# Kernel optimization log

Hardware: AMD Instinct MI355X
Metric: run time of the kernel (lower is better)

The kernel has to match this reference:

```python
import jax, jax.numpy as jnp
import numpy as np

NEG = -1e9  # matches torch masked_fill value -1000000000.0


def setup_inputs() -> dict:
    key = jax.random.key(0)
    ks = jax.random.split(key, 8)
    B, n, m, d = 16, 1024, 128, 768
    C = jax.random.normal(ks[0], (B, n, d), jnp.float32)
    Q = jax.random.normal(ks[1], (B, m, d), jnp.float32)
    c_mask = jax.random.randint(ks[2], (B, 1, n), 0, 2).astype(bool)
    q_mask = jax.random.randint(ks[3], (B, 1, m), 0, 2).astype(bool)
    w1 = jax.random.normal(ks[4], (d,), jnp.float32)
    w2 = jax.random.normal(ks[5], (d,), jnp.float32)
    w3 = jax.random.normal(ks[6], (1, 1, d), jnp.float32)
    bias = jax.random.normal(ks[7], (1, 1), jnp.float32)
    return {"C": C, "Q": Q, "c_mask": c_mask, "q_mask": q_mask,
            "w1": w1, "w2": w2, "w3": w3, "bias": bias}


def reference(C, Q, c_mask, q_mask, w1, w2, w3, bias):
    # trilinear score S[b,i,j] = w1.C_i + w2.Q_j + (C_i * w3) . Q_j
    c_logit = jnp.einsum('bnd,d->bn', C, w1)[:, :, None]      # [B,n,1]
    q_logit = jnp.einsum('bmd,d->bm', Q, w2)[:, None, :]      # [B,1,m]
    dot_logit = jnp.einsum('bnd,bmd->bnm', C * w3, Q)         # [B,n,m]
    S = c_logit + q_logit + dot_logit                          # [B,n,m]

    # C2Q: mask padded query cols and padded context rows, softmax over query dim
    Sm = jnp.where(q_mask, NEG, S)                             # q_mask [B,1,m]
    Sm = jnp.where(jnp.swapaxes(c_mask, 1, 2), NEG, Sm)        # c_mask^T [B,n,1]
    C2Q = jax.nn.softmax(Sm, axis=-1)                          # [B,n,m]

    # Q2C: mask context cols of S^T, max over query dim, softmax over context dim
    St = jnp.where(c_mask, NEG, jnp.swapaxes(S, 1, 2))         # [B,m,n]
    q2c_logits = jnp.max(St, axis=1, keepdims=True)            # [B,1,n]
    Q2C = jax.nn.softmax(q2c_logits, axis=-1)                  # [B,1,n]

    A = jnp.einsum('bnm,bmd->bnd', C2Q, Q)                     # [B,n,d]
    # torch expands Q2C to [B,n,n] then bmm's with C; every row is identical,
    # so compute once and broadcast: [B,1,n] @ [B,n,d] -> [B,1,d]
    Bctx = jnp.einsum('bon,bnd->bod', Q2C, C)                  # [B,1,d]
    Bfull = jnp.broadcast_to(Bctx, C.shape)
    out = jnp.concatenate([C, A, C * A, C * Bfull], axis=-1)   # [B,n,4d]
    return out
```

## Files before the change

kernel.cpp:

```cpp
#include <hip/hip_runtime.h>
#include <math.h>
#include <stdint.h>

#define NEGV -1e9f
typedef float f32x4 __attribute__((ext_vector_type(4)));
typedef short bf16x8 __attribute__((ext_vector_type(8)));
typedef unsigned int u32x4 __attribute__((ext_vector_type(4)));

constexpr int B_ = 16, N_ = 1024, M_ = 128, D_ = 768;
constexpr int NCH = 12;

constexpr size_t OFF_QLOGP  = 0;
constexpr size_t OFF_BCTX   = 98304;
constexpr size_t OFF_PART   = 147456;
constexpr size_t OFF_ROWMAX = 147456;
constexpr size_t OFF_WQ2C   = 212992;
constexpr size_t OFF_PIMG   = 2244608;
constexpr size_t OFF_QIMG   = 10633216;
constexpr size_t SZ_QIMG    = 3145728;
constexpr size_t WS_NEED    = OFF_QIMG + 4 * SZ_QIMG;

__device__ __forceinline__ unsigned short bf_rne(float x) {
    unsigned u = __float_as_uint(x);
    return (unsigned short)((u + 0x7fffu + ((u >> 16) & 1u)) >> 16);
}
__device__ __forceinline__ void splitf(float x, unsigned short& h, unsigned short& l) {
    unsigned short hb = bf_rne(x);
    float hf = __uint_as_float((unsigned)hb << 16);
    h = hb;
    l = bf_rne(x - hf);
}
__device__ __forceinline__ void gl_lds16(const void* g, void* l) {
    __builtin_amdgcn_global_load_lds(
        (const __attribute__((address_space(1))) void*)g,
        (__attribute__((address_space(3))) void*)l, 16, 0, 0);
}

__global__ __launch_bounds__(256) void k_prep(const float* __restrict__ Q,
                                              const float* __restrict__ w2,
                                              const float* __restrict__ w3,
                                              char* __restrict__ qwh, char* __restrict__ qwl,
                                              char* __restrict__ qth, char* __restrict__ qtl,
                                              float* __restrict__ qlogp) {
    int b = blockIdx.x / NCH, c = blockIdx.x % NCH;
    int t = threadIdx.x;
    __shared__ unsigned sT[128][66];
    __shared__ float sW2[64], sW3c[64];
    if (t < 64) sW2[t] = w2[c * 64 + t];
    else if (t < 128) sW3c[t - 64] = w3[c * 64 + (t - 64)];
    __syncthreads();
    int j = t >> 1, half = t & 1;
    const float* src = Q + ((size_t)(b * M_ + j)) * D_ + c * 64 + half * 32;
    unsigned short hs[32], ls[32];
    float qsum = 0.f;
#pragma unroll
    for (int u = 0; u < 8; ++u) {
        float4 v = *(const float4*)(src + u * 4);
        float f[4] = {v.x, v.y, v.z, v.w};
#pragma unroll
        for (int e = 0; e < 4; ++e) {
            int idx = u * 4 + e, d = half * 32 + idx;
            qsum += f[e] * sW2[d];
            unsigned short rh, rl; splitf(f[e], rh, rl);
            sT[j][d] = ((unsigned)rh << 16) | (unsigned)rl;
            unsigned short h, l; splitf(f[e] * sW3c[d], h, l);
            hs[idx] = h; ls[idx] = l;
        }
    }
    qsum += __shfl_xor(qsum, 1);
    if (half == 0) qlogp[(size_t)(b * M_ + j) * NCH + c] = qsum;
    size_t cb = ((size_t)(b * NCH + c)) * 16384;
    {
        int jh = j >> 6, jt = (j >> 4) & 3, c15j = j & 15;
#pragma unroll
        for (int u2 = 0; u2 < 4; ++u2) {
            int g = half * 4 + u2, ks = g >> 2, q4g = g & 3;
            int lane = q4g * 16 + c15j;
            bf16x8 hv, lv;
#pragma unroll
            for (int e = 0; e < 8; ++e) { hv[e] = (short)hs[u2 * 8 + e]; lv[e] = (short)ls[u2 * 8 + e]; }
            size_t off = cb + (size_t)((((jh * 2 + ks) * 4 + jt) * 64 + lane) * 16);
            *(bf16x8*)(qwh + off) = hv;
            *(bf16x8*)(qwl + off) = lv;
        }
    }
    __syncthreads();
#pragma unroll
    for (int u = 0; u < 4; ++u) {
        int id = t * 4 + u;
        int dd = id >> 4, gj = id & 15;
        int jh3 = dd >> 5, dt = (dd >> 4) & 1, c15q = dd & 15;
        int ks2 = gj >> 2, q4g = gj & 3;
        int lane = q4g * 16 + c15q;
        bf16x8 hv, lv;
#pragma unroll
        for (int e = 0; e < 8; ++e) {
            unsigned p = sT[gj * 8 + e][dd];
            hv[e] = (short)(p >> 16); lv[e] = (short)(p & 0xffffu);
        }
        size_t off = cb + (size_t)((((jh3 * 4 + ks2) * 2 + dt) * 64 + lane) * 16);
        *(bf16x8*)(qth + off) = hv;
        *(bf16x8*)(qtl + off) = lv;
    }
}

__global__ __launch_bounds__(256, 3) void k_main1(const float* __restrict__ C,
                                                  const int* __restrict__ c_mask,
                                                  const int* __restrict__ q_mask,
                                                  const float* __restrict__ w1,
                                                  const float* __restrict__ qlogp,
                                                  const char* __restrict__ qwh,
                                                  const char* __restrict__ qwl,
                                                  float* __restrict__ part,
                                                  char* __restrict__ pimg) {
    const int bid = (blockIdx.x & 7) * 64 + (blockIdx.x >> 3);
    const int b  = bid >> 5;
    const int r0 = (bid & 31) * 32;
    const int t  = threadIdx.x;
    const int wv = t >> 6, lane = t & 63;
    const int rg = wv >> 1, jh = wv & 1;
    const int q4 = lane >> 4, c15 = t & 15;

    const float* Cb = C + ((size_t)(b * N_ + r0)) * D_;

    __shared__ __align__(16) char uni[49152];
    __shared__ float sQlog[M_];
    __shared__ int   sQmask[M_];
    __shared__ float sClog[32], sMraw[32], sMl[32], sWr[32];
    __shared__ float sRedR[64], sRedM[64], sRedS[64];

    char* sQH = uni;
    char* sQL = uni + 16384;
    char* sPH = uni + 32768;
    char* sPL = uni + 40960;
    float* sW1 = (float*)(uni + 32768);

    for (int k = t; k < D_; k += 256) sW1[k] = w1[k];
    if (t < M_) {
        const float* qp = qlogp + (size_t)(b * M_ + t) * NCH;
        float4 x = *(const float4*)qp, y = *(const float4*)(qp + 4), z = *(const float4*)(qp + 8);
        sQlog[t] = ((x.x + x.y) + (x.z + x.w)) + ((y.x + y.y) + (y.z + y.w)) +
                   ((z.x + z.y) + (z.z + z.w));
        sQmask[t] = q_mask[b * M_ + t];
    }
    __syncthreads();

    f32x4 acc[4] = {};
    float clogp = 0.f;
    const int arow = rg * 16 + c15;
    const float* CbA = Cb + (size_t)arow * D_;
    const size_t qcb = (size_t)(b * NCH) * 16384;

    for (int kidx = 0; kidx < NCH; ++kidx) {
        __syncthreads();
        {
            size_t gb = qcb + (size_t)kidx * 16384;
#pragma unroll
            for (int it = 0; it < 4; ++it) {
                int qo = it * 4096 + wv * 1024;
                gl_lds16(qwh + gb + qo + lane * 16, sQH + qo);
                gl_lds16(qwl + gb + qo + lane * 16, sQL + qo);
            }
        }
        bf16x8 ah[2], al[2];
        const int kb = kidx * 64;
#pragma unroll
        for (int ks = 0; ks < 2; ++ks) {
            const int k0 = kb + (ks * 4 + q4) * 8;
            float4 ca  = *(const float4*)(CbA + k0);
            float4 cb2 = *(const float4*)(CbA + k0 + 4);
            float cc[8] = {ca.x, ca.y, ca.z, ca.w, cb2.x, cb2.y, cb2.z, cb2.w};
#pragma unroll
            for (int e = 0; e < 8; ++e) {
                clogp += cc[e] * sW1[k0 + e];
                unsigned short h, l; splitf(cc[e], h, l);
                ah[ks][e] = (short)h; al[ks][e] = (short)l;
            }
        }
        __syncthreads();
#pragma unroll
        for (int ks = 0; ks < 2; ++ks) {
#pragma unroll
            for (int jt = 0; jt < 4; ++jt) {
                int fo = (((jh * 2 + ks) * 4 + jt) * 64 + lane) * 16;
                bf16x8 bh = *(const bf16x8*)(sQH + fo);
                bf16x8 bl = *(const bf16x8*)(sQL + fo);
                acc[jt] = __builtin_amdgcn_mfma_f32_16x16x32_bf16(ah[ks], bh, acc[jt], 0, 0, 0);
                acc[jt] = __builtin_amdgcn_mfma_f32_16x16x32_bf16(ah[ks], bl, acc[jt], 0, 0, 0);
                acc[jt] = __builtin_amdgcn_mfma_f32_16x16x32_bf16(al[ks], bh, acc[jt], 0, 0, 0);
            }
        }
    }
    clogp += __shfl_xor(clogp, 16);
    clogp += __shfl_xor(clogp, 32);
    if (jh == 0 && q4 == 0) sClog[arow] = clogp;
    __syncthreads();

    float qlg[4]; int qmv[4];
#pragma unroll
    for (int jt = 0; jt < 4; ++jt) {
        int j = jh * 64 + jt * 16 + c15;
        qlg[jt] = sQlog[j]; qmv[jt] = sQmask[j];
    }
    int cmv[4]; float clgr[4];
#pragma unroll
    for (int rr = 0; rr < 4; ++rr) {
        int row = rg * 16 + q4 * 4 + rr;
        cmv[rr]  = c_mask[b * N_ + r0 + row];
        clgr[rr] = sClog[row];
    }
    float mv[4][4], rmx[4], mmx[4];
#pragma unroll
    for (int rr = 0; rr < 4; ++rr) { rmx[rr] = -INFINITY; mmx[rr] = -INFINITY; }
#pragma unroll
    for (int jt = 0; jt < 4; ++jt)
#pragma unroll
        for (int rr = 0; rr < 4; ++rr) {
            float val = acc[jt][rr] + clgr[rr] + qlg[jt];
            float m   = (cmv[rr] | qmv[jt]) ? NEGV : val;
            mv[jt][rr] = m;
            rmx[rr] = fmaxf(rmx[rr], val);
            mmx[rr] = fmaxf(mmx[rr], m);
        }
#pragma unroll
    for (int rr = 0; rr < 4; ++rr)
// ... 20 lines not shown
        if (jh == 0 && c15 == 0) sMraw[row] = Mraw;
        sum[rr] = 0.f;
    }
    float p[4][4];
#pragma unroll
    for (int jt = 0; jt < 4; ++jt)
#pragma unroll
        for (int rr = 0; rr < 4; ++rr) {
            float e = __expf(mv[jt][rr] - Mm[rr]);
            p[jt][rr] = e; sum[rr] += e;
        }
#pragma unroll
    for (int rr = 0; rr < 4; ++rr) {
#pragma unroll
        for (int off = 8; off; off >>= 1) sum[rr] += __shfl_xor(sum[rr], off);
        if (c15 == 0) sRedS[(rg * 16 + q4 * 4 + rr) * 2 + jh] = sum[rr];
    }
    __syncthreads();
#pragma unroll
    for (int rr = 0; rr < 4; ++rr) {
        int row = rg * 16 + q4 * 4 + rr;
        float inv = 1.f / (sRedS[row * 2] + sRedS[row * 2 + 1]);
#pragma unroll
        for (int jt = 0; jt < 4; ++jt) {
            float P = p[jt][rr] * inv;
            unsigned short h, l; splitf(P, h, l);
            int j = jh * 64 + jt * 16 + c15;
            int addr = row * 256 + (((j >> 3) ^ (row & 7)) * 16) + (j & 7) * 2;
            *(short*)(sPH + addr) = (short)h;
            *(short*)(sPL + addr) = (short)l;
        }
    }
    __syncthreads();

    if (t < 32) sMl[t] = (c_mask[b * N_ + r0 + t] != 0) ? NEGV : sMraw[t];
    __syncthreads();
    float lm = -INFINITY;
#pragma unroll
    for (int r = 0; r < 32; ++r) lm = fmaxf(lm, sMl[r]);
    if (t < 32) sWr[t] = __expf(sMl[t] - lm);
    __syncthreads();
    float den = 0.f;
#pragma unroll
    for (int r = 0; r < 32; ++r) den += sWr[r];
    {
        float a0 = 0.f, a1 = 0.f, a2 = 0.f;
        for (int r = 0; r < 32; ++r) {
            float w = sWr[r];
            if (w != 0.f) {
                const float* cr = Cb + (size_t)r * D_;
                a0 += w * cr[t]; a1 += w * cr[t + 256]; a2 += w * cr[t + 512];
            }
        }
        float* slot = part + (size_t)bid * 1024;
        slot[2 + t] = a0; slot[2 + t + 256] = a1; slot[2 + t + 512] = a2;
        if (t == 0) { slot[0] = lm; slot[1] = den; }
    }
#pragma unroll
    for (int i = 0; i < 2; ++i) {
        *(u32x4*)(pimg + (size_t)bid * 16384 + t * 32 + i * 16) =
            *(const u32x4*)(sPH + t * 32 + i * 16);
        *(u32x4*)(pimg + (size_t)bid * 16384 + 8192 + t * 32 + i * 16) =
            *(const u32x4*)(sPL + t * 32 + i * 16);
    }
}

__global__ __launch_bounds__(256, 3) void k_main2(const float* __restrict__ C,
                                                  const float* __restrict__ part,
                                                  const char* __restrict__ qth,
                                                  const char* __restrict__ qtl,
                                                  const char* __restrict__ pimg,
                                                  float* __restrict__ out) {
    const int bid = (blockIdx.x & 7) * 64 + (blockIdx.x >> 3);
    const int b  = bid >> 5;
    const int r0 = (bid & 31) * 32;
    const int t  = threadIdx.x;
    const int wv = t >> 6, lane = t & 63;
    const int rg = wv >> 1, jh = wv & 1;
    const int q4 = lane >> 4, c15 = t & 15;

    const float* Cb = C + ((size_t)(b * N_ + r0)) * D_;

    __shared__ __align__(16) char uni[49152];
    __shared__ float sBctx[D_];
    __shared__ float sLm[32], sDen[32], sSc[32];
    char* sQtH = uni;
    char* sQtL = uni + 16384;
    char* sPH  = uni + 32768;
    char* sPL  = uni + 40960;

    {
        const char* ps = pimg + (size_t)bid * 16384;
#pragma unroll
        for (int it = 0; it < 2; ++it) {
            int off = it * 4096 + wv * 1024;
            gl_lds16(ps + off + lane * 16, sPH + off);
            gl_lds16(ps + 8192 + off + lane * 16, sPL + off);
        }
    }
    if (t < 32) {
        const float* s = part + (size_t)(b * 32 + t) * 1024;
        sLm[t] = s[0]; sDen[t] = s[1];
    }
    __syncthreads();
    {
        float gm = -INFINITY;
#pragma unroll
        for (int r = 0; r < 32; ++r) gm = fmaxf(gm, sLm[r]);
        if (t < 32) sSc[t] = __expf(sLm[t] - gm);
        __syncthreads();
        float Ds = 0.f;
#pragma unroll
        for (int r = 0; r < 32; ++r) Ds += sDen[r] * sSc[r];
        float inv = 1.f / Ds;
#pragma unroll
        for (int u = 0; u < 3; ++u) {
            int col = t + u * 256;
            float a = 0.f;
            for (int rt = 0; rt < 32; ++rt)
                a += sSc[rt] * part[(size_t)(b * 32 + rt) * 1024 + 2 + col];
            sBctx[col] = a * inv;
        }
    }
    __syncthreads();

    bf16x8 pah[4], pal[4];
    const int prow = rg * 16 + c15;
#pragma unroll
    for (int ks2 = 0; ks2 < 4; ++ks2) {
        int gja = ks2 * 4 + q4;
        int pgp = (gja ^ (prow & 7)) * 16;
        pah[ks2] = *(const bf16x8*)(sPH + prow * 256 + pgp);
        pal[ks2] = *(const bf16x8*)(sPL + prow * 256 + pgp);
    }

    const size_t qcb = (size_t)(b * NCH) * 16384;
    for (int dc = 0; dc < NCH; ++dc) {
        __syncthreads();
        {
            size_t gb = qcb + (size_t)dc * 16384;
#pragma unroll
            for (int it = 0; it < 4; ++it) {
                int qo = it * 4096 + wv * 1024;
                gl_lds16(qth + gb + qo + lane * 16, sQtH + qo);
                gl_lds16(qtl + gb + qo + lane * 16, sQtL + qo);
            }
        }
        float cpre[2][4], gpre[2];
#pragma unroll
        for (int dt = 0; dt < 2; ++dt) {
            int dcol = dc * 64 + jh * 32 + dt * 16 + c15;
            gpre[dt] = sBctx[dcol];
#pragma unroll
            for (int rr = 0; rr < 4; ++rr) {
                int row = rg * 16 + q4 * 4 + rr;
                cpre[dt][rr] = Cb[(size_t)row * D_ + dcol];
            }
        }
        __syncthreads();
        f32x4 acc2[2] = {};
#pragma unroll
        for (int ks2 = 0; ks2 < 4; ++ks2) {
#pragma unroll
            for (int dt = 0; dt < 2; ++dt) {
                int fo = (((jh * 4 + ks2) * 2 + dt) * 64 + lane) * 16;
                bf16x8 bh = *(const bf16x8*)(sQtH + fo);
                bf16x8 bl = *(const bf16x8*)(sQtL + fo);
                acc2[dt] = __builtin_amdgcn_mfma_f32_16x16x32_bf16(pah[ks2], bh, acc2[dt], 0, 0, 0);
                acc2[dt] = __builtin_amdgcn_mfma_f32_16x16x32_bf16(pah[ks2], bl, acc2[dt], 0, 0, 0);
                acc2[dt] = __builtin_amdgcn_mfma_f32_16x16x32_bf16(pal[ks2], bh, acc2[dt], 0, 0, 0);
            }
        }
#pragma unroll
        for (int dt = 0; dt < 2; ++dt) {
            int dcol = dc * 64 + jh * 32 + dt * 16 + c15;
            float g = gpre[dt];
#pragma unroll
            for (int rr = 0; rr < 4; ++rr) {
                int row = rg * 16 + q4 * 4 + rr;
                float a = acc2[dt][rr];
                float c = cpre[dt][rr];
                size_t ob = (size_t)(b * N_ + r0 + row) * 3072;
                out[ob + dcol] = c;
                out[ob + 768 + dcol] = a;
                out[ob + 1536 + dcol] = c * a;
                out[ob + 2304 + dcol] = c * g;
            }
        }
    }
}

__global__ __launch_bounds__(256) void k_qlogit(const float* __restrict__ Q,
                                                const float* __restrict__ w2,
                                                float* __restrict__ qlog) {
    int idx  = blockIdx.x * 4 + (threadIdx.x >> 6);
    int lane = threadIdx.x & 63;
    const float* q = Q + (size_t)idx * D_;
    float s = 0.f;
    for (int k = lane; k < D_; k += 64) s += q[k] * w2[k];
#pragma unroll
    for (int off = 32; off; off >>= 1) s += __shfl_xor(s, off);
    if (lane == 0) qlog[idx] = s;
}

__global__ __launch_bounds__(256, 2) void k_main_fb(const float* __restrict__ C,
                                                    const float* __restrict__ Q,
                                                    const int* __restrict__ c_mask,
                                                    const int* __restrict__ q_mask,
                                                    const float* __restrict__ w1,
                                                    const float* __restrict__ w3,
                                                    const float* __restrict__ qlog,
                                                    float* __restrict__ rowmax,
                                                    float* __restrict__ out) {
    const int bid = (blockIdx.x & 7) * 64 + (blockIdx.x >> 3);
    const int b  = bid >> 5;
    const int r0 = (bid & 31) * 32;
    const int t  = threadIdx.x;
    const int wv = t >> 6;
    const int rg = wv >> 1, jh = wv & 1;
    const int q4 = (t & 63) >> 4, c15 = t & 15;

    const float* Cb = C + ((size_t)(b * N_ + r0)) * D_;
    const float* Qb = Q + (size_t)b * M_ * D_;

    __shared__ __align__(16) char uni[49152];
    __shared__ float sW1[D_], sW3[D_];
    __shared__ float sQlog[M_];
    __shared__ int   sQmask[M_];
    __shared__ float sClog[32];
    __shared__ float sRedR[64], sRedM[64], sRedS[64];

    char* sCwH = uni;
    char* sCwL = uni + 4096;
    char* sQH  = uni + 8192;
    char* sQL  = uni + 24576;
    char* sPt  = uni;
    char* sQtP = uni + 16384;

    for (int k = t; k < D_; k += 256) { sW1[k] = w1[k]; sW3[k] = w3[k]; }
    if (t < M_) { sQlog[t] = qlog[b * M_ + t]; sQmask[t] = q_mask[b * M_ + t]; }

    f32x4 acc[4] = {};
    float clog = 0.f;
    const int cr = t >> 3, ckq = t & 7;
    const int qj = t >> 1, qk0 = (t & 1) * 32;

    for (int kb = 0; kb < D_; kb += 64) {
        __syncthreads();
        {
            const float* p = Cb + (size_t)cr * D_ + kb + ckq * 8;
            float4 a  = *(const float4*)p;
            float4 bb = *(const float4*)(p + 4);
            float cc[8] = {a.x, a.y, a.z, a.w, bb.x, bb.y, bb.z, bb.w};
            bf16x8 hv, lv;
            int kk = kb + ckq * 8;
#pragma unroll
            for (int e = 0; e < 8; ++e) {
                clog += cc[e] * sW1[kk + e];
                unsigned short h, l;
                splitf(cc[e] * sW3[kk + e], h, l);
                hv[e] = (short)h; lv[e] = (short)l;
            }
            int pg = (ckq ^ (cr & 7)) * 16;
            *(bf16x8*)(sCwH + cr * 128 + pg) = hv;
            *(bf16x8*)(sCwL + cr * 128 + pg) = lv;
        }
        {
            const float* p = Qb + (size_t)qj * D_ + kb + qk0;
#pragma unroll
            for (int u = 0; u < 4; ++u) {
// ... 140 lines not shown
        __syncthreads();
        f32x4 acc2[2] = {};
        const int prow = rg * 16 + c15;
#pragma unroll
        for (int ks2 = 0; ks2 < 4; ++ks2) {
            int gu0 = ks2 * 8 + q4 * 2;
            u32x4 pa = *(const u32x4*)(sPt + prow * 512 + ((gu0 ^ (c15 & 7)) * 16));
            u32x4 pb = *(const u32x4*)(sPt + prow * 512 + (((gu0 + 1) ^ (c15 & 7)) * 16));
            bf16x8 phi, plo;
#pragma unroll
            for (int e = 0; e < 4; ++e) {
                phi[e]     = (short)(pa[e] >> 16); plo[e]     = (short)(pa[e] & 0xffffu);
                phi[e + 4] = (short)(pb[e] >> 16); plo[e + 4] = (short)(pb[e] & 0xffffu);
            }
#pragma unroll
            for (int dt = 0; dt < 2; ++dt) {
                int dr = jh * 32 + dt * 16 + c15;
                u32x4 qa = *(const u32x4*)(sQtP + dr * 512 + ((gu0 ^ (dr & 7)) * 16));
                u32x4 qb = *(const u32x4*)(sQtP + dr * 512 + (((gu0 + 1) ^ (dr & 7)) * 16));
                bf16x8 bh, bl;
#pragma unroll
                for (int e = 0; e < 4; ++e) {
                    bh[e]     = (short)(qa[e] >> 16); bl[e]     = (short)(qa[e] & 0xffffu);
                    bh[e + 4] = (short)(qb[e] >> 16); bl[e + 4] = (short)(qb[e] & 0xffffu);
                }
                acc2[dt] = __builtin_amdgcn_mfma_f32_16x16x32_bf16(phi, bh, acc2[dt], 0, 0, 0);
                acc2[dt] = __builtin_amdgcn_mfma_f32_16x16x32_bf16(phi, bl, acc2[dt], 0, 0, 0);
                acc2[dt] = __builtin_amdgcn_mfma_f32_16x16x32_bf16(plo, bh, acc2[dt], 0, 0, 0);
            }
        }
#pragma unroll
        for (int dt = 0; dt < 2; ++dt)
#pragma unroll
            for (int rr = 0; rr < 4; ++rr) {
                int row  = rg * 16 + q4 * 4 + rr;
                int dcol = d0 + jh * 32 + dt * 16 + c15;
                float a = acc2[dt][rr];
                float c = Cb[(size_t)row * D_ + dcol];
                size_t ob = (size_t)(b * N_ + r0 + row) * 3072;
                out[ob + dcol] = c;
                out[ob + 768 + dcol] = a;
                out[ob + 1536 + dcol] = c * a;
            }
    }
}

__global__ __launch_bounds__(256) void k_q2c(const float* __restrict__ rowmax,
                                             const int* __restrict__ c_mask,
                                             float* __restrict__ wq2c) {
    int b = blockIdx.x, t = threadIdx.x;
    __shared__ float red[8];
    float l[4];
#pragma unroll
    for (int u = 0; u < 4; ++u) {
        int i = t + u * 256;
        l[u] = (c_mask[b * N_ + i] != 0) ? NEGV : rowmax[b * N_ + i];
    }
    float mx = fmaxf(fmaxf(l[0], l[1]), fmaxf(l[2], l[3]));
#pragma unroll
    for (int off = 32; off; off >>= 1) mx = fmaxf(mx, __shfl_xor(mx, off));
    if ((t & 63) == 0) red[t >> 6] = mx;
    __syncthreads();
    mx = fmaxf(fmaxf(red[0], red[1]), fmaxf(red[2], red[3]));
    float e[4], s = 0.f;
#pragma unroll
    for (int u = 0; u < 4; ++u) { e[u] = __expf(l[u] - mx); s += e[u]; }
#pragma unroll
    for (int off = 32; off; off >>= 1) s += __shfl_xor(s, off);
    if ((t & 63) == 0) red[4 + (t >> 6)] = s;
    __syncthreads();
    s = red[4] + red[5] + red[6] + red[7];
    float inv = 1.f / s;
#pragma unroll
    for (int u = 0; u < 4; ++u) wq2c[b * N_ + t + u * 256] = e[u] * inv;
}

__global__ __launch_bounds__(256) void k_bctx(const float* __restrict__ C,
                                              const float* __restrict__ wq2c,
                                              float* __restrict__ Bctx) {
    int b  = blockIdx.x / 12;
    int c0 = (blockIdx.x % 12) * 64;
    int t  = threadIdx.x;
    int col = t & 63, ig = t >> 6;
    __shared__ float part[4][64];
    const float* wb = wq2c + b * N_;
    const float* Cb = C + (size_t)b * N_ * D_;
    float s = 0.f;
    for (int i = ig * 256; i < ig * 256 + 256; ++i)
        s += wb[i] * Cb[(size_t)i * D_ + c0 + col];
    part[ig][col] = s;
    __syncthreads();
    if (t < 64) Bctx[b * D_ + c0 + t] = part[0][t] + part[1][t] + part[2][t] + part[3][t];
}

__global__ __launch_bounds__(192) void k_final(const float* __restrict__ C,
                                               const float* __restrict__ Bctx,
                                               float* __restrict__ out) {
    int row = blockIdx.x;
    int b = row >> 10;
    int t = threadIdx.x;
    float4 c = *(const float4*)(C + (size_t)row * D_ + t * 4);
    float4 g = *(const float4*)(Bctx + (size_t)b * D_ + t * 4);
    *(float4*)(out + (size_t)row * 3072 + 2304 + t * 4) =
        make_float4(c.x * g.x, c.y * g.y, c.z * g.z, c.w * g.w);
}

extern "C" void kernel_launch(void* const* d_in, const int* in_sizes, int n_in,
                              void* d_out, int out_size, void* d_ws, size_t ws_size,
                              hipStream_t stream) {
    const float* C      = (const float*)d_in[0];
    const float* Q      = (const float*)d_in[1];
    const int*   c_mask = (const int*)d_in[2];
    const int*   q_mask = (const int*)d_in[3];
    const float* w1     = (const float*)d_in[4];
    const float* w2     = (const float*)d_in[5];
    const float* w3     = (const float*)d_in[6];
    float* out = (float*)d_out;
    char*  wsb = (char*)d_ws;

    float* qlogp  = (float*)(wsb + OFF_QLOGP);
    float* part   = (float*)(wsb + OFF_PART);
    char*  pimg   = wsb + OFF_PIMG;

    if (ws_size >= WS_NEED) {
        char* qwh = wsb + OFF_QIMG;
        char* qwl = qwh + SZ_QIMG;
        char* qth = qwl + SZ_QIMG;
        char* qtl = qth + SZ_QIMG;
        k_prep<<<B_ * NCH, 256, 0, stream>>>(Q, w2, w3, qwh, qwl, qth, qtl, qlogp);
        k_main1<<<512, 256, 0, stream>>>(C, c_mask, q_mask, w1, qlogp, qwh, qwl, part, pimg);
        k_main2<<<512, 256, 0, stream>>>(C, part, qth, qtl, pimg, out);
    } else {
        float* qlog   = (float*)(wsb + OFF_QLOGP);
        float* rowmax = (float*)(wsb + OFF_ROWMAX);
        float* wq2c   = (float*)(wsb + OFF_WQ2C);
        float* bctx   = (float*)(wsb + OFF_BCTX);
        k_qlogit<<<512, 256, 0, stream>>>(Q, w2, qlog);
        k_main_fb<<<512, 256, 0, stream>>>(C, Q, c_mask, q_mask, w1, w3, qlog, rowmax, out);
        k_q2c<<<16, 256, 0, stream>>>(rowmax, c_mask, wq2c);
        k_bctx<<<192, 256, 0, stream>>>(C, wq2c, bctx);
        k_final<<<16384, 192, 0, stream>>>(C, bctx, out);
    }
}
```

Measured before the change: 94.77 us.

## Fuse main1 and main2 into one cooperative kernel with grid sync

Merges the two main kernels into a single cooperative launch. The probability matrix stays in registers instead of going through a workspace image, and a grid-wide sync replaces the kernel boundary for the Q2C reduction. The prep kernel is split into twice as many blocks, each handling half a column chunk, to raise parallelism. This removes a launch and the P image round trip, but adds a grid barrier and needs all 512 blocks resident at once; if that fails it falls back to the two-kernel path.

```diff
diff --git a/kernel.cpp b/kernel.cpp
--- a/kernel.cpp
+++ b/kernel.cpp
@@ -1,6 +1,9 @@
 #include <hip/hip_runtime.h>
+#include <hip/hip_cooperative_groups.h>
 #include <math.h>
 #include <stdint.h>
+
+namespace cg = cooperative_groups;
 
 #define NEGV -1e9f
 typedef float f32x4 __attribute__((ext_vector_type(4)));
@@ -9,16 +12,14 @@
 
 constexpr int B_ = 16, N_ = 1024, M_ = 128, D_ = 768;
 constexpr int NCH = 12;
-
-constexpr size_t OFF_QLOGP  = 0;
-constexpr size_t OFF_BCTX   = 98304;
-constexpr size_t OFF_PART   = 147456;
-constexpr size_t OFF_ROWMAX = 147456;
-constexpr size_t OFF_WQ2C   = 212992;
-constexpr size_t OFF_PIMG   = 2244608;
-constexpr size_t OFF_QIMG   = 10633216;
-constexpr size_t SZ_QIMG    = 3145728;
-constexpr size_t WS_NEED    = OFF_QIMG + 4 * SZ_QIMG;
+constexpr int NQP = 24;
+
+constexpr size_t OFF_QLOGP = 0;
+constexpr size_t OFF_PART  = 196608;
+constexpr size_t OFF_PIMG  = 2293760;
+constexpr size_t OFF_QIMG  = 10682368;
+constexpr size_t SZ_QIMG   = 3145728;
+constexpr size_t WS_NEED   = OFF_QIMG + 4 * SZ_QIMG;
 
 __device__ __forceinline__ unsigned short bf_rne(float x) {
     unsigned u = __float_as_uint(x);
@@ -36,45 +37,48 @@
         (__attribute__((address_space(3))) void*)l, 16, 0, 0);
 }
 
-__global__ __launch_bounds__(256) void k_prep(const float* __restrict__ Q,
-                                              const float* __restrict__ w2,
-                                              const float* __restrict__ w3,
-                                              char* __restrict__ qwh, char* __restrict__ qwl,
-                                              char* __restrict__ qth, char* __restrict__ qtl,
-                                              float* __restrict__ qlogp) {
-    int b = blockIdx.x / NCH, c = blockIdx.x % NCH;
-    int t = threadIdx.x;
-    __shared__ unsigned sT[128][66];
-    __shared__ float sW2[64], sW3c[64];
-    if (t < 64) sW2[t] = w2[c * 64 + t];
-    else if (t < 128) sW3c[t - 64] = w3[c * 64 + (t - 64)];
-    __syncthreads();
-    int j = t >> 1, half = t & 1;
-    const float* src = Q + ((size_t)(b * M_ + j)) * D_ + c * 64 + half * 32;
-    unsigned short hs[32], ls[32];
+__global__ __launch_bounds__(256) void k_prep2(const float* __restrict__ Q,
+                                               const float* __restrict__ w2,
+                                               const float* __restrict__ w3,
+                                               char* __restrict__ qwh, char* __restrict__ qwl,
+                                               char* __restrict__ qth, char* __restrict__ qtl,
+                                               float* __restrict__ qlogp) {
+    const int bi = blockIdx.x;
+    const int b = bi / (NCH * 2), rem = bi % (NCH * 2);
+    const int c = rem >> 1, half = rem & 1;
+    const int t = threadIdx.x;
+    __shared__ unsigned sT[128][33];
+    __shared__ float sW2h[32], sW3h[32];
+    if (t < 32) sW2h[t] = w2[c * 64 + half * 32 + t];
+    else if (t < 64) sW3h[t - 32] = w3[c * 64 + half * 32 + (t - 32)];
+    __syncthreads();
+    const int j = t >> 1, h16 = t & 1;
+    const float* src = Q + ((size_t)(b * M_ + j)) * D_ + c * 64 + half * 32 + h16 * 16;
+    unsigned short hs[16], ls[16];
     float qsum = 0.f;
 #pragma unroll
-    for (int u = 0; u < 8; ++u) {
+    for (int u = 0; u < 4; ++u) {
         float4 v = *(const float4*)(src + u * 4);
         float f[4] = {v.x, v.y, v.z, v.w};
 #pragma unroll
         for (int e = 0; e < 4; ++e) {
-            int idx = u * 4 + e, d = half * 32 + idx;
-            qsum += f[e] * sW2[d];
+            int idx = u * 4 + e;
+            int lc  = h16 * 16 + idx;
+            qsum += f[e] * sW2h[lc];
             unsigned short rh, rl; splitf(f[e], rh, rl);
-            sT[j][d] = ((unsigned)rh << 16) | (unsigned)rl;
-            unsigned short h, l; splitf(f[e] * sW3c[d], h, l);
+            sT[j][lc] = ((unsigned)rh << 16) | (unsigned)rl;
+            unsigned short h, l; splitf(f[e] * sW3h[lc], h, l);
             hs[idx] = h; ls[idx] = l;
         }
     }
     qsum += __shfl_xor(qsum, 1);
-    if (half == 0) qlogp[(size_t)(b * M_ + j) * NCH + c] = qsum;
+    if (h16 == 0) qlogp[(size_t)(b * M_ + j) * NQP + c * 2 + half] = qsum;
     size_t cb = ((size_t)(b * NCH + c)) * 16384;
     {
         int jh = j >> 6, jt = (j >> 4) & 3, c15j = j & 15;
 #pragma unroll
-        for (int u2 = 0; u2 < 4; ++u2) {
-            int g = half * 4 + u2, ks = g >> 2, q4g = g & 3;
+        for (int u2 = 0; u2 < 2; ++u2) {
+            int g = half * 4 + h16 * 2 + u2, ks = g >> 2, q4g = g & 3;
             int lane = q4g * 16 + c15j;
             bf16x8 hv, lv;
 #pragma unroll
@@ -86,21 +90,324 @@
     }
     __syncthreads();
 #pragma unroll
-    for (int u = 0; u < 4; ++u) {
-        int id = t * 4 + u;
-        int dd = id >> 4, gj = id & 15;
-        int jh3 = dd >> 5, dt = (dd >> 4) & 1, c15q = dd & 15;
+    for (int u = 0; u < 2; ++u) {
+        int id = t * 2 + u;
+        int dd_loc = id >> 4, gj = id & 15;
+        int dt = dd_loc >> 4, c15q = dd_loc & 15;
         int ks2 = gj >> 2, q4g = gj & 3;
         int lane = q4g * 16 + c15q;
         bf16x8 hv, lv;
 #pragma unroll
         for (int e = 0; e < 8; ++e) {
-            unsigned p = sT[gj * 8 + e][dd];
+            unsigned p = sT[gj * 8 + e][dd_loc];
             hv[e] = (short)(p >> 16); lv[e] = (short)(p & 0xffffu);
         }
-        size_t off = cb + (size_t)((((jh3 * 4 + ks2) * 2 + dt) * 64 + lane) * 16);
+        size_t off = cb + (size_t)((((half * 4 + ks2) * 2 + dt) * 64 + lane) * 16);
         *(bf16x8*)(qth + off) = hv;
         *(bf16x8*)(qtl + off) = lv;
+    }
+}
+
+__global__ __launch_bounds__(256, 3) void k_mainc(const float* __restrict__ C,
+                                                  const int* __restrict__ c_mask,
+                                                  const int* __restrict__ q_mask,
+                                                  const float* __restrict__ w1,
+                                                  const float* __restrict__ qlogp,
+                                                  const char* __restrict__ qwh,
+                                                  const char* __restrict__ qwl,
+                                                  const char* __restrict__ qth,
+                                                  const char* __restrict__ qtl,
+                                                  float* __restrict__ part,
+                                                  float* __restrict__ out) {
+    cg::grid_group grid = cg::this_grid();
+    const int bid = (blockIdx.x & 7) * 64 + (blockIdx.x >> 3);
+    const int b  = bid >> 5;
+    const int r0 = (bid & 31) * 32;
+    const int t  = threadIdx.x;
+    const int wv = t >> 6, lane = t & 63;
+    const int rg = wv >> 1, jh = wv & 1;
+    const int q4 = lane >> 4, c15 = t & 15;
+
+    const float* Cb = C + ((size_t)(b * N_ + r0)) * D_;
+
+    __shared__ __align__(16) char uni[49152];
+    __shared__ float sQlog[M_];
+    __shared__ int   sQmask[M_];
+    __shared__ float sClog[32], sMraw[32], sMl[32], sWr[32];
+    __shared__ float sRedR[64], sRedM[64], sRedS[64];
+    __shared__ float sLm[32], sDen[32], sSc[32];
+
+    char*  sQH   = uni;
+    char*  sQL   = uni + 16384;
+    char*  sPH   = uni + 32768;
+    char*  sPL   = uni + 40960;
+    float* sW1   = (float*)(uni + 32768);
+    float* sBctx = (float*)(uni + 32768);
+    char*  sQtH  = uni;
+    char*  sQtL  = uni + 16384;
+
+    for (int k = t; k < D_; k += 256) sW1[k] = w1[k];
+    if (t < M_) {
+        const float* qp = qlogp + (size_t)(b * M_ + t) * NQP;
+        float s = 0.f;
+#pragma unroll
+        for (int u = 0; u < 6; ++u) {
+            float4 v = ((const float4*)qp)[u];
+            s += (v.x + v.y) + (v.z + v.w);
+        }
+        sQlog[t] = s;
+        sQmask[t] = q_mask[b * M_ + t];
+    }
+    __syncthreads();
+
+    f32x4 acc[4] = {};
+    float clogp = 0.f;
+    const int arow = rg * 16 + c15;
+    const float* CbA = Cb + (size_t)arow * D_;
+    const size_t qcb = (size_t)(b * NCH) * 16384;
+
+    for (int kidx = 0; kidx < NCH; ++kidx) {
+        __syncthreads();
+        {
+            size_t gb = qcb + (size_t)kidx * 16384;
+#pragma unroll
+            for (int it = 0; it < 4; ++it) {
+                int qo = it * 4096 + wv * 1024;
+                gl_lds16(qwh + gb + qo + lane * 16, sQH + qo);
+                gl_lds16(qwl + gb + qo + lane * 16, sQL + qo);
+            }
+        }
+        bf16x8 ah[2], al[2];
+        const int kb = kidx * 64;
+#pragma unroll
+        for (int ks = 0; ks < 2; ++ks) {
+            const int k0 = kb + (ks * 4 + q4) * 8;
+            float4 ca  = *(const float4*)(CbA + k0);
+            float4 cb2 = *(const float4*)(CbA + k0 + 4);
+            float cc[8] = {ca.x, ca.y, ca.z, ca.w, cb2.x, cb2.y, cb2.z, cb2.w};
+#pragma unroll
+            for (int e = 0; e < 8; ++e) {
+                clogp += cc[e] * sW1[k0 + e];
+                unsigned short h, l; splitf(cc[e], h, l);
+                ah[ks][e] = (short)h; al[ks][e] = (short)l;
+            }
+        }
+        __syncthreads();
+#pragma unroll
+        for (int ks = 0; ks < 2; ++ks) {
+#pragma unroll
+            for (int jt = 0; jt < 4; ++jt) {
+                int fo = (((jh * 2 + ks) * 4 + jt) * 64 + lane) * 16;
+                bf16x8 bh = *(const bf16x8*)(sQH + fo);
+                bf16x8 bl = *(const bf16x8*)(sQL + fo);
+                acc[jt] = __builtin_amdgcn_mfma_f32_16x16x32_bf16(ah[ks], bh, acc[jt], 0, 0, 0);
+                acc[jt] = __builtin_amdgcn_mfma_f32_16x16x32_bf16(ah[ks], bl, acc[jt], 0, 0, 0);
+                acc[jt] = __builtin_amdgcn_mfma_f32_16x16x32_bf16(al[ks], bh, acc[jt], 0, 0, 0);
+            }
+        }
+    }
+    clogp += __shfl_xor(clogp, 16);
+    clogp += __shfl_xor(clogp, 32);
+    if (jh == 0 && q4 == 0) sClog[arow] = clogp;
+    __syncthreads();
+
+    float qlg[4]; int qmv[4];
+#pragma unroll
+    for (int jt = 0; jt < 4; ++jt) {
+        int j = jh * 64 + jt * 16 + c15;
+        qlg[jt] = sQlog[j]; qmv[jt] = sQmask[j];
+    }
+    int cmv[4]; float clgr[4];
+#pragma unroll
+    for (int rr = 0; rr < 4; ++rr) {
+        int row = rg * 16 + q4 * 4 + rr;
+        cmv[rr]  = c_mask[b * N_ + r0 + row];
+        clgr[rr] = sClog[row];
+    }
+    float mv[4][4], rmx[4], mmx[4];
+#pragma unroll
+    for (int rr = 0; rr < 4; ++rr) { rmx[rr] = -INFINITY; mmx[rr] = -INFINITY; }
+#pragma unroll
+    for (int jt = 0; jt < 4; ++jt)
+#pragma unroll
+        for (int rr = 0; rr < 4; ++rr) {
+            float val = acc[jt][rr] + clgr[rr] + qlg[jt];
+            float m   = (cmv[rr] | qmv[jt]) ? NEGV : val;
+            mv[jt][rr] = m;
+            rmx[rr] = fmaxf(rmx[rr], val);
+            mmx[rr] = fmaxf(mmx[rr], m);
+        }
+#pragma unroll
+    for (int rr = 0; rr < 4; ++rr)
+#pragma unroll
+        for (int off = 8; off; off >>= 1) {
+            rmx[rr] = fmaxf(rmx[rr], __shfl_xor(rmx[rr], off));
+            mmx[rr] = fmaxf(mmx[rr], __shfl_xor(mmx[rr], off));
+        }
+    if (c15 == 0) {
+#pragma unroll
+        for (int rr = 0; rr < 4; ++rr) {
+            int row = rg * 16 + q4 * 4 + rr;
+            sRedR[row * 2 + jh] = rmx[rr];
+            sRedM[row * 2 + jh] = mmx[rr];
+        }
+    }
+    __syncthreads();
+    float Mm[4], sum[4];
+#pragma unroll
+    for (int rr = 0; rr < 4; ++rr) {
+        int row = rg * 16 + q4 * 4 + rr;
+        float Mraw = fmaxf(sRedR[row * 2], sRedR[row * 2 + 1]);
+        Mm[rr] = fmaxf(sRedM[row * 2], sRedM[row * 2 + 1]);
+        if (jh == 0 && c15 == 0) sMraw[row] = Mraw;
+        sum[rr] = 0.f;
+    }
+    float p[4][4];
+#pragma unroll
+    for (int jt = 0; jt < 4; ++jt)
+#pragma unroll
+        for (int rr = 0; rr < 4; ++rr) {
+            float e = __expf(mv[jt][rr] - Mm[rr]);
+            p[jt][rr] = e; sum[rr] += e;
+        }
+#pragma unroll
+    for (int rr = 0; rr < 4; ++rr) {
+#pragma unroll
+        for (int off = 8; off; off >>= 1) sum[rr] += __shfl_xor(sum[rr], off);
+        if (c15 == 0) sRedS[(rg * 16 + q4 * 4 + rr) * 2 + jh] = sum[rr];
+    }
+    __syncthreads();
+#pragma unroll
+    for (int rr = 0; rr < 4; ++rr) {
+        int row = rg * 16 + q4 * 4 + rr;
+        float inv = 1.f / (sRedS[row * 2] + sRedS[row * 2 + 1]);
+#pragma unroll
+        for (int jt = 0; jt < 4; ++jt) {
+            float P = p[jt][rr] * inv;
+            unsigned short h, l; splitf(P, h, l);
+            int j = jh * 64 + jt * 16 + c15;
+            int addr = row * 256 + (((j >> 3) ^ (row & 7)) * 16) + (j & 7) * 2;
+            *(short*)(sPH + addr) = (short)h;
+            *(short*)(sPL + addr) = (short)l;
+        }
+    }
+    __syncthreads();
+
+    bf16x8 pah[4], pal[4];
+    const int prow = rg * 16 + c15;
+#pragma unroll
+    for (int ks2 = 0; ks2 < 4; ++ks2) {
+        int gja = ks2 * 4 + q4;
+        int pgp = (gja ^ (prow & 7)) * 16;
+        pah[ks2] = *(const bf16x8*)(sPH + prow * 256 + pgp);
+        pal[ks2] = *(const bf16x8*)(sPL + prow * 256 + pgp);
+    }
+
+    if (t < 32) sMl[t] = (c_mask[b * N_ + r0 + t] != 0) ? NEGV : sMraw[t];
+    __syncthreads();
+    float lm = -INFINITY;
+#pragma unroll
+    for (int r = 0; r < 32; ++r) lm = fmaxf(lm, sMl[r]);
+    if (t < 32) sWr[t] = __expf(sMl[t] - lm);
+    __syncthreads();
+    float den = 0.f;
+#pragma unroll
+    for (int r = 0; r < 32; ++r) den += sWr[r];
+    {
+        float a0 = 0.f, a1 = 0.f, a2 = 0.f;
+        for (int r = 0; r < 32; ++r) {
+            float w = sWr[r];
+            if (w != 0.f) {
+                const float* cr = Cb + (size_t)r * D_;
+                a0 += w * cr[t]; a1 += w * cr[t + 256]; a2 += w * cr[t + 512];
+            }
+        }
+        float* slot = part + (size_t)bid * 1024;
+        slot[2 + t] = a0; slot[2 + t + 256] = a1; slot[2 + t + 512] = a2;
+        if (t == 0) { slot[0] = lm; slot[1] = den; }
+    }
+    __threadfence();
+    grid.sync();
+
+    if (t < 32) {
+        const float* s = part + (size_t)(b * 32 + t) * 1024;
+        sLm[t] = s[0]; sDen[t] = s[1];
+    }
+    __syncthreads();
+    {
+        float gm = -INFINITY;
+#pragma unroll
+        for (int r = 0; r < 32; ++r) gm = fmaxf(gm, sLm[r]);
+        if (t < 32) sSc[t] = __expf(sLm[t] - gm);
+        __syncthreads();
+        float Ds = 0.f;
+#pragma unroll
+        for (int r = 0; r < 32; ++r) Ds += sDen[r] * sSc[r];
+        float inv = 1.f / Ds;
+#pragma unroll
+        for (int u = 0; u < 3; ++u) {
+            int col = t + u * 256;
+            float a = 0.f;
+            for (int rt = 0; rt < 32; ++rt)
+                a += sSc[rt] * part[(size_t)(b * 32 + rt) * 1024 + 2 + col];
+            sBctx[col] = a * inv;
+        }
+    }
+    __syncthreads();
+
+    const size_t qcb3 = (size_t)(b * NCH) * 16384;
+    for (int dc = 0; dc < NCH; ++dc) {
+        __syncthreads();
+        {
+            size_t gb = qcb3 + (size_t)dc * 16384;
+#pragma unroll
+            for (int it = 0; it < 4; ++it) {
+                int qo = it * 4096 + wv * 1024;
+                gl_lds16(qth + gb + qo + lane * 16, sQtH + qo);
+                gl_lds16(qtl + gb + qo + lane * 16, sQtL + qo);
+            }
+        }
+        float cpre[2][4], gpre[2];
+#pragma unroll
+        for (int dt = 0; dt < 2; ++dt) {
+            int dcol = dc * 64 + jh * 32 + dt * 16 + c15;
+            gpre[dt] = sBctx[dcol];
+#pragma unroll
+            for (int rr = 0; rr < 4; ++rr) {
+                int row = rg * 16 + q4 * 4 + rr;
+                cpre[dt][rr] = Cb[(size_t)row * D_ + dcol];
+            }
+        }
+        __syncthreads();
+        f32x4 acc2[2] = {};
+#pragma unroll
+        for (int ks2 = 0; ks2 < 4; ++ks2) {
+#pragma unroll
+            for (int dt = 0; dt < 2; ++dt) {
+                int fo = (((jh * 4 + ks2) * 2 + dt) * 64 + lane) * 16;
+                bf16x8 bh = *(const bf16x8*)(sQtH + fo);
+                bf16x8 bl = *(const bf16x8*)(sQtL + fo);
+                acc2[dt] = __builtin_amdgcn_mfma_f32_16x16x32_bf16(pah[ks2], bh, acc2[dt], 0, 0, 0);
+                acc2[dt] = __builtin_amdgcn_mfma_f32_16x16x32_bf16(pah[ks2], bl, acc2[dt], 0, 0, 0);
+                acc2[dt] = __builtin_amdgcn_mfma_f32_16x16x32_bf16(pal[ks2], bh, acc2[dt], 0, 0, 0);
+            }
+        }
+#pragma unroll
+        for (int dt = 0; dt < 2; ++dt) {
+            int dcol = dc * 64 + jh * 32 + dt * 16 + c15;
+            float g = gpre[dt];
+#pragma unroll
+            for (int rr = 0; rr < 4; ++rr) {
+                int row = rg * 16 + q4 * 4 + rr;
+                float a = acc2[dt][rr];
+                float c = cpre[dt][rr];
+                size_t ob = (size_t)(b * N_ + r0 + row) * 3072;
+                out[ob + dcol] = c;
+                out[ob + 768 + dcol] = a;
+                out[ob + 1536 + dcol] = c * a;
+                out[ob + 2304 + dcol] = c * g;
+            }
+        }
     }
 }
 
@@ -137,10 +444,14 @@
 
     for (int k = t; k < D_; k += 256) sW1[k] = w1[k];
     if (t < M_) {
-        const float* qp = qlogp + (size_t)(b * M_ + t) * NCH;
-        float4 x = *(const float4*)qp, y = *(const float4*)(qp + 4), z = *(const float4*)(qp + 8);
-        sQlog[t] = ((x.x + x.y) + (x.z + x.w)) + ((y.x + y.y) + (y.z + y.w)) +
-                   ((z.x + z.y) + (z.z + z.w));
+        const float* qp = qlogp + (size_t)(b * M_ + t) * NQP;
+        float s = 0.f;
+#pragma unroll
+        for (int u = 0; u < 6; ++u) {
+            float4 v = ((const float4*)qp)[u];
+            s += (v.x + v.y) + (v.z + v.w);
+        }
+        sQlog[t] = s;
         sQmask[t] = q_mask[b * M_ + t];
     }
     __syncthreads();
@@ -737,15 +1048,15 @@
     int c0 = (blockIdx.x % 12) * 64;
     int t  = threadIdx.x;
     int col = t & 63, ig = t >> 6;
-    __shared__ float part[4][64];
+    __shared__ float partl[4][64];
     const float* wb = wq2c + b * N_;
     const float* Cb = C + (size_t)b * N_ * D_;
     float s = 0.f;
     for (int i = ig * 256; i < ig * 256 + 256; ++i)
         s += wb[i] * Cb[(size_t)i * D_ + c0 + col];
-    part[ig][col] = s;
-    __syncthreads();
-    if (t < 64) Bctx[b * D_ + c0 + t] = part[0][t] + part[1][t] + part[2][t] + part[3][t];
+    partl[ig][col] = s;
+    __syncthreads();
+    if (t < 64) Bctx[b * D_ + c0 + t] = partl[0][t] + partl[1][t] + partl[2][t] + partl[3][t];
 }
 
 __global__ __launch_bounds__(192) void k_final(const float* __restrict__ C,
@@ -773,23 +1084,31 @@
     float* out = (float*)d_out;
     char*  wsb = (char*)d_ws;
 
-    float* qlogp  = (float*)(wsb + OFF_QLOGP);
-    float* part   = (float*)(wsb + OFF_PART);
-    char*  pimg   = wsb + OFF_PIMG;
+    float* qlogp = (float*)(wsb + OFF_QLOGP);
+    float* part  = (float*)(wsb + OFF_PART);
+    char*  pimg  = wsb + OFF_PIMG;
 
     if (ws_size >= WS_NEED) {
         char* qwh = wsb + OFF_QIMG;
         char* qwl = qwh + SZ_QIMG;
         char* qth = qwl + SZ_QIMG;
         char* qtl = qth + SZ_QIMG;
-        k_prep<<<B_ * NCH, 256, 0, stream>>>(Q, w2, w3, qwh, qwl, qth, qtl, qlogp);
-        k_main1<<<512, 256, 0, stream>>>(C, c_mask, q_mask, w1, qlogp, qwh, qwl, part, pimg);
-        k_main2<<<512, 256, 0, stream>>>(C, part, qth, qtl, pimg, out);
+        k_prep2<<<B_ * NCH * 2, 256, 0, stream>>>(Q, w2, w3, qwh, qwl, qth, qtl, qlogp);
+        const char *qwh_c = qwh, *qwl_c = qwl, *qth_c = qth, *qtl_c = qtl;
+        void* args[11] = {(void*)&C, (void*)&c_mask, (void*)&q_mask, (void*)&w1,
+                          (void*)&qlogp, (void*)&qwh_c, (void*)&qwl_c, (void*)&qth_c,
+                          (void*)&qtl_c, (void*)&part, (void*)&out};
+        hipError_t e = hipLaunchCooperativeKernel((void*)k_mainc, dim3(512), dim3(256),
+                                                  args, 0, stream);
+        if (e != hipSuccess) {
+            k_main1<<<512, 256, 0, stream>>>(C, c_mask, q_mask, w1, qlogp, qwh, qwl, part, pimg);
+            k_main2<<<512, 256, 0, stream>>>(C, part, qth, qtl, pimg, out);
+        }
     } else {
-        float* qlog   = (float*)(wsb + OFF_QLOGP);
-        float* rowmax = (float*)(wsb + OFF_ROWMAX);
-        float* wq2c   = (float*)(wsb + OFF_WQ2C);
-        float* bctx   = (float*)(wsb + OFF_BCTX);
+        float* qlog   = (float*)(wsb + 0);
+        float* rowmax = (float*)(wsb + 196608);
+        float* wq2c   = (float*)(wsb + 262144);
+        float* bctx   = (float*)(wsb + 327680);
         k_qlogit<<<512, 256, 0, stream>>>(Q, w2, qlog);
         k_main_fb<<<512, 256, 0, stream>>>(C, Q, c_mask, q_mask, w1, w3, qlog, rowmax, out);
         k_q2c<<<16, 256, 0, stream>>>(rowmax, c_mask, wq2c);
```

Result: slower. 217.5 us (+129.5%).

## Vectorize k_main2 output stores via lane shuffles and split prep blocks

Applied to the files above, without the earlier changes.

In k_main2, the MFMA accumulator values are transposed across lanes with xor shuffles, so each thread owns four consecutive columns of one row. The C loads and the four output-segment writes then become float4 accesses instead of scalar strided ones, aiming to cut memory transaction count on the large output write. The prep kernel is also split into twice as many blocks, each handling half a chunk, with the q-logit partials widened to 24 per row. The extra shuffles and select logic add ALU work in exchange for wider memory accesses.

```diff
diff --git a/kernel.cpp b/kernel.cpp
--- a/kernel.cpp
+++ b/kernel.cpp
@@ -9,16 +9,14 @@
 
 constexpr int B_ = 16, N_ = 1024, M_ = 128, D_ = 768;
 constexpr int NCH = 12;
-
-constexpr size_t OFF_QLOGP  = 0;
-constexpr size_t OFF_BCTX   = 98304;
-constexpr size_t OFF_PART   = 147456;
-constexpr size_t OFF_ROWMAX = 147456;
-constexpr size_t OFF_WQ2C   = 212992;
-constexpr size_t OFF_PIMG   = 2244608;
-constexpr size_t OFF_QIMG   = 10633216;
-constexpr size_t SZ_QIMG    = 3145728;
-constexpr size_t WS_NEED    = OFF_QIMG + 4 * SZ_QIMG;
+constexpr int NQP = 24;
+
+constexpr size_t OFF_QLOGP = 0;
+constexpr size_t OFF_PART  = 196608;
+constexpr size_t OFF_PIMG  = 2293760;
+constexpr size_t OFF_QIMG  = 10682368;
+constexpr size_t SZ_QIMG   = 3145728;
+constexpr size_t WS_NEED   = OFF_QIMG + 4 * SZ_QIMG;
 
 __device__ __forceinline__ unsigned short bf_rne(float x) {
     unsigned u = __float_as_uint(x);
@@ -36,45 +34,48 @@
         (__attribute__((address_space(3))) void*)l, 16, 0, 0);
 }
 
-__global__ __launch_bounds__(256) void k_prep(const float* __restrict__ Q,
-                                              const float* __restrict__ w2,
-                                              const float* __restrict__ w3,
-                                              char* __restrict__ qwh, char* __restrict__ qwl,
-                                              char* __restrict__ qth, char* __restrict__ qtl,
-                                              float* __restrict__ qlogp) {
-    int b = blockIdx.x / NCH, c = blockIdx.x % NCH;
-    int t = threadIdx.x;
-    __shared__ unsigned sT[128][66];
-    __shared__ float sW2[64], sW3c[64];
-    if (t < 64) sW2[t] = w2[c * 64 + t];
-    else if (t < 128) sW3c[t - 64] = w3[c * 64 + (t - 64)];
-    __syncthreads();
-    int j = t >> 1, half = t & 1;
-    const float* src = Q + ((size_t)(b * M_ + j)) * D_ + c * 64 + half * 32;
-    unsigned short hs[32], ls[32];
+__global__ __launch_bounds__(256) void k_prep2(const float* __restrict__ Q,
+                                               const float* __restrict__ w2,
+                                               const float* __restrict__ w3,
+                                               char* __restrict__ qwh, char* __restrict__ qwl,
+                                               char* __restrict__ qth, char* __restrict__ qtl,
+                                               float* __restrict__ qlogp) {
+    const int bi = blockIdx.x;
+    const int b = bi / (NCH * 2), rem = bi % (NCH * 2);
+    const int c = rem >> 1, half = rem & 1;
+    const int t = threadIdx.x;
+    __shared__ unsigned sT[128][33];
+    __shared__ float sW2h[32], sW3h[32];
+    if (t < 32) sW2h[t] = w2[c * 64 + half * 32 + t];
+    else if (t < 64) sW3h[t - 32] = w3[c * 64 + half * 32 + (t - 32)];
+    __syncthreads();
+    const int j = t >> 1, h16 = t & 1;
+    const float* src = Q + ((size_t)(b * M_ + j)) * D_ + c * 64 + half * 32 + h16 * 16;
+    unsigned short hs[16], ls[16];
     float qsum = 0.f;
 #pragma unroll
-    for (int u = 0; u < 8; ++u) {
+    for (int u = 0; u < 4; ++u) {
         float4 v = *(const float4*)(src + u * 4);
         float f[4] = {v.x, v.y, v.z, v.w};
 #pragma unroll
         for (int e = 0; e < 4; ++e) {
-            int idx = u * 4 + e, d = half * 32 + idx;
-            qsum += f[e] * sW2[d];
+            int idx = u * 4 + e;
+            int lc  = h16 * 16 + idx;
+            qsum += f[e] * sW2h[lc];
             unsigned short rh, rl; splitf(f[e], rh, rl);
-            sT[j][d] = ((unsigned)rh << 16) | (unsigned)rl;
-            unsigned short h, l; splitf(f[e] * sW3c[d], h, l);
+            sT[j][lc] = ((unsigned)rh << 16) | (unsigned)rl;
+            unsigned short h, l; splitf(f[e] * sW3h[lc], h, l);
             hs[idx] = h; ls[idx] = l;
         }
     }
     qsum += __shfl_xor(qsum, 1);
-    if (half == 0) qlogp[(size_t)(b * M_ + j) * NCH + c] = qsum;
+    if (h16 == 0) qlogp[(size_t)(b * M_ + j) * NQP + c * 2 + half] = qsum;
     size_t cb = ((size_t)(b * NCH + c)) * 16384;
     {
         int jh = j >> 6, jt = (j >> 4) & 3, c15j = j & 15;
 #pragma unroll
-        for (int u2 = 0; u2 < 4; ++u2) {
-            int g = half * 4 + u2, ks = g >> 2, q4g = g & 3;
+        for (int u2 = 0; u2 < 2; ++u2) {
+            int g = half * 4 + h16 * 2 + u2, ks = g >> 2, q4g = g & 3;
             int lane = q4g * 16 + c15j;
             bf16x8 hv, lv;
 #pragma unroll
@@ -86,19 +87,19 @@
     }
     __syncthreads();
 #pragma unroll
-    for (int u = 0; u < 4; ++u) {
-        int id = t * 4 + u;
-        int dd = id >> 4, gj = id & 15;
-        int jh3 = dd >> 5, dt = (dd >> 4) & 1, c15q = dd & 15;
+    for (int u = 0; u < 2; ++u) {
+        int id = t * 2 + u;
+        int dd_loc = id >> 4, gj = id & 15;
+        int dt = dd_loc >> 4, c15q = dd_loc & 15;
         int ks2 = gj >> 2, q4g = gj & 3;
         int lane = q4g * 16 + c15q;
         bf16x8 hv, lv;
 #pragma unroll
         for (int e = 0; e < 8; ++e) {
-            unsigned p = sT[gj * 8 + e][dd];
+            unsigned p = sT[gj * 8 + e][dd_loc];
             hv[e] = (short)(p >> 16); lv[e] = (short)(p & 0xffffu);
         }
-        size_t off = cb + (size_t)((((jh3 * 4 + ks2) * 2 + dt) * 64 + lane) * 16);
+        size_t off = cb + (size_t)((((half * 4 + ks2) * 2 + dt) * 64 + lane) * 16);
         *(bf16x8*)(qth + off) = hv;
         *(bf16x8*)(qtl + off) = lv;
     }
@@ -137,10 +138,14 @@
 
     for (int k = t; k < D_; k += 256) sW1[k] = w1[k];
     if (t < M_) {
-        const float* qp = qlogp + (size_t)(b * M_ + t) * NCH;
-        float4 x = *(const float4*)qp, y = *(const float4*)(qp + 4), z = *(const float4*)(qp + 8);
-        sQlog[t] = ((x.x + x.y) + (x.z + x.w)) + ((y.x + y.y) + (y.z + y.w)) +
-                   ((z.x + z.y) + (z.z + z.w));
+        const float* qp = qlogp + (size_t)(b * M_ + t) * NQP;
+        float s = 0.f;
+#pragma unroll
+        for (int u = 0; u < 6; ++u) {
+            float4 v = ((const float4*)qp)[u];
+            s += (v.x + v.y) + (v.z + v.w);
+        }
+        sQlog[t] = s;
         sQmask[t] = q_mask[b * M_ + t];
     }
     __syncthreads();
@@ -327,7 +332,7 @@
     const float* Cb = C + ((size_t)(b * N_ + r0)) * D_;
 
     __shared__ __align__(16) char uni[49152];
-    __shared__ float sBctx[D_];
+    __shared__ __align__(16) float sBctx[D_];
     __shared__ float sLm[32], sDen[32], sSc[32];
     char* sQtH = uni;
     char* sQtL = uni + 16384;
@@ -379,7 +384,11 @@
         pal[ks2] = *(const bf16x8*)(sPL + prow * 256 + pgp);
     }
 
+    const int trow = rg * 16 + q4 * 4 + (c15 & 3);
+    const int tg4  = (c15 >> 2) * 4;
+    const int a2   = t & 3;
     const size_t qcb = (size_t)(b * NCH) * 16384;
+
     for (int dc = 0; dc < NCH; ++dc) {
         __syncthreads();
         {
@@ -391,16 +400,12 @@
                 gl_lds16(qtl + gb + qo + lane * 16, sQtL + qo);
             }
         }
-        float cpre[2][4], gpre[2];
+        float4 cpre[2], gpre[2];
 #pragma unroll
         for (int dt = 0; dt < 2; ++dt) {
-            int dcol = dc * 64 + jh * 32 + dt * 16 + c15;
-            gpre[dt] = sBctx[dcol];
-#pragma unroll
-            for (int rr = 0; rr < 4; ++rr) {
-                int row = rg * 16 + q4 * 4 + rr;
-                cpre[dt][rr] = Cb[(size_t)row * D_ + dcol];
-            }
+            int col4 = dc * 64 + jh * 32 + dt * 16 + tg4;
+            cpre[dt] = *(const float4*)(Cb + (size_t)trow * D_ + col4);
+            gpre[dt] = *(const float4*)&sBctx[col4];
         }
         __syncthreads();
         f32x4 acc2[2] = {};
@@ -418,19 +423,24 @@
         }
 #pragma unroll
         for (int dt = 0; dt < 2; ++dt) {
-            int dcol = dc * 64 + jh * 32 + dt * 16 + c15;
-            float g = gpre[dt];
-#pragma unroll
-            for (int rr = 0; rr < 4; ++rr) {
-                int row = rg * 16 + q4 * 4 + rr;
-                float a = acc2[dt][rr];
-                float c = cpre[dt][rr];
-                size_t ob = (size_t)(b * N_ + r0 + row) * 3072;
-                out[ob + dcol] = c;
-                out[ob + 768 + dcol] = a;
-                out[ob + 1536 + dcol] = c * a;
-                out[ob + 2304 + dcol] = c * g;
-            }
+            float v0 = acc2[dt][0], v1 = acc2[dt][1], v2 = acc2[dt][2], v3 = acc2[dt][3];
+            {
+                float t0 = __shfl_xor(v1, 1), t1 = __shfl_xor(v0, 1);
+                float t2 = __shfl_xor(v3, 1), t3 = __shfl_xor(v2, 1);
+                if (a2 & 1) { v0 = t0; v2 = t2; } else { v1 = t1; v3 = t3; }
+            }
+            {
+                float t0 = __shfl_xor(v2, 2), t1 = __shfl_xor(v3, 2);
+                float t2 = __shfl_xor(v0, 2), t3 = __shfl_xor(v1, 2);
+                if (a2 & 2) { v0 = t0; v1 = t1; } else { v2 = t2; v3 = t3; }
+            }
+            int col4 = dc * 64 + jh * 32 + dt * 16 + tg4;
+            float4 cv = cpre[dt], gv = gpre[dt];
+            size_t ob = (size_t)(b * N_ + r0 + trow) * 3072;
+            *(float4*)(out + ob + col4)        = cv;
+            *(float4*)(out + ob + 768 + col4)  = make_float4(v0, v1, v2, v3);
+            *(float4*)(out + ob + 1536 + col4) = make_float4(cv.x * v0, cv.y * v1, cv.z * v2, cv.w * v3);
+            *(float4*)(out + ob + 2304 + col4) = make_float4(cv.x * gv.x, cv.y * gv.y, cv.z * gv.z, cv.w * gv.w);
         }
     }
 }
@@ -737,15 +747,15 @@
     int c0 = (blockIdx.x % 12) * 64;
     int t  = threadIdx.x;
     int col = t & 63, ig = t >> 6;
-    __shared__ float part[4][64];
+    __shared__ float partl[4][64];
     const float* wb = wq2c + b * N_;
     const float* Cb = C + (size_t)b * N_ * D_;
     float s = 0.f;
     for (int i = ig * 256; i < ig * 256 + 256; ++i)
         s += wb[i] * Cb[(size_t)i * D_ + c0 + col];
-    part[ig][col] = s;
-    __syncthreads();
-    if (t < 64) Bctx[b * D_ + c0 + t] = part[0][t] + part[1][t] + part[2][t] + part[3][t];
+    partl[ig][col] = s;
+    __syncthreads();
+    if (t < 64) Bctx[b * D_ + c0 + t] = partl[0][t] + partl[1][t] + partl[2][t] + partl[3][t];
 }
 
 __global__ __launch_bounds__(192) void k_final(const float* __restrict__ C,
@@ -773,23 +783,23 @@
     float* out = (float*)d_out;
     char*  wsb = (char*)d_ws;
 
-    float* qlogp  = (float*)(wsb + OFF_QLOGP);
-    float* part   = (float*)(wsb + OFF_PART);
-    char*  pimg   = wsb + OFF_PIMG;
+    float* qlogp = (float*)(wsb + OFF_QLOGP);
+    float* part  = (float*)(wsb + OFF_PART);
+    char*  pimg  = wsb + OFF_PIMG;
 
     if (ws_size >= WS_NEED) {
         char* qwh = wsb + OFF_QIMG;
         char* qwl = qwh + SZ_QIMG;
         char* qth = qwl + SZ_QIMG;
         char* qtl = qth + SZ_QIMG;
-        k_prep<<<B_ * NCH, 256, 0, stream>>>(Q, w2, w3, qwh, qwl, qth, qtl, qlogp);
+        k_prep2<<<B_ * NCH * 2, 256, 0, stream>>>(Q, w2, w3, qwh, qwl, qth, qtl, qlogp);
         k_main1<<<512, 256, 0, stream>>>(C, c_mask, q_mask, w1, qlogp, qwh, qwl, part, pimg);
         k_main2<<<512, 256, 0, stream>>>(C, part, qth, qtl, pimg, out);
     } else {
-        float* qlog   = (float*)(wsb + OFF_QLOGP);
-        float* rowmax = (float*)(wsb + OFF_ROWMAX);
-        float* wq2c   = (float*)(wsb + OFF_WQ2C);
-        float* bctx   = (float*)(wsb + OFF_BCTX);
+        float* qlog   = (float*)(wsb + 0);
+        float* rowmax = (float*)(wsb + 196608);
+        float* wq2c   = (float*)(wsb + 262144);
+        float* bctx   = (float*)(wsb + 327680);
         k_qlogit<<<512, 256, 0, stream>>>(Q, w2, qlog);
         k_main_fb<<<512, 256, 0, stream>>>(C, Q, c_mask, q_mask, w1, w3, qlog, rowmax, out);
         k_q2c<<<16, 256, 0, stream>>>(rowmax, c_mask, wq2c);
```

After: 102.4 us. +8.0%, slower.
